# Kernel optimization log

Hardware: AMD Instinct MI355X
Metric: run time of the kernel (lower is better)

Reference implementation:

```python
import jax, jax.numpy as jnp
import numpy as np

N_M, N_D, E, D, H, O = 50000, 20000, 600000, 128, 128, 64


def _graph_conv(x_src, x_dst, src, dst, W_rel, b_rel, W_root, ew=None):
    # PyG GraphConv: lin_rel(scatter_add(msg)) + lin_root(x_dst)
    msg = x_src[src]                       # [E, d_src] gather
    if ew is not None:
        msg = msg * ew[:, None]            # edge-weighted messages
    agg = jax.ops.segment_sum(msg, dst, num_segments=x_dst.shape[0])  # [N_dst, d_src]
    return agg @ W_rel + b_rel + x_dst @ W_root


def setup_inputs() -> dict:
    key = jax.random.key(0)
    ks = jax.random.split(key, 16)
    s = 1.0 / np.sqrt(D)
    inp = {
        "x_meas": jax.random.normal(ks[0], (N_M, D), jnp.float32),
        "x_dem": jax.random.normal(ks[1], (N_D, D), jnp.float32),
        "src_m": jax.random.randint(ks[2], (E,), 0, N_M, jnp.int32),
        "dst_m": jax.random.randint(ks[3], (E,), 0, N_M, jnp.int32),
        "src_b": jax.random.randint(ks[4], (E,), 0, N_M, jnp.int32),
        "dst_b": jax.random.randint(ks[5], (E,), 0, N_D, jnp.int32),
        "edge_weight": jax.random.normal(ks[6], (E,), jnp.float32),
        "W_rel1": jax.random.normal(ks[7], (D, H), jnp.float32) * s,
        "b_rel1": jnp.zeros((H,), jnp.float32),
        "W_root1": jax.random.normal(ks[8], (D, H), jnp.float32) * s,
        "W_rel2": jax.random.normal(ks[9], (D, H), jnp.float32) * s,
        "b_rel2": jnp.zeros((H,), jnp.float32),
        "W_root2": jax.random.normal(ks[10], (D, H), jnp.float32) * s,
        "W_rel3": jax.random.normal(ks[11], (H, H), jnp.float32) * s,
        "b_rel3": jnp.zeros((H,), jnp.float32),
        "W_root3": jax.random.normal(ks[12], (H, H), jnp.float32) * s,
        "W_lin": jax.random.normal(ks[13], (H, O), jnp.float32) * (1.0 / np.sqrt(H)),
        "b_lin": jnp.zeros((O,), jnp.float32),
    }
    return inp


def reference(x_meas, x_dem, src_m, dst_m, src_b, dst_b, edge_weight,
              W_rel1, b_rel1, W_root1, W_rel2, b_rel2, W_root2,
              W_rel3, b_rel3, W_root3, W_lin, b_lin):
    ew = jax.nn.sigmoid(edge_weight)
    movie_x = jax.nn.relu(_graph_conv(x_meas, x_meas, src_m, dst_m, W_rel1, b_rel1, W_root1))
    user_x = jax.nn.relu(_graph_conv(x_meas, x_dem, src_b, dst_b, W_rel2, b_rel2, W_root2, ew))
    user_x = jax.nn.relu(_graph_conv(movie_x, user_x, src_b, dst_b, W_rel3, b_rel3, W_root3, ew))
    return user_x @ W_lin + b_lin  # [N_D, O]
```

## Files before the change

### kernel.cpp

```cpp
#include <hip/hip_runtime.h>


typedef unsigned short u16;
typedef unsigned int u32;
typedef __attribute__((ext_vector_type(8))) short bf16x8;
typedef __attribute__((ext_vector_type(4))) float f32x4;

#define NMC 50000
#define NDC 20000
#define EC  600000
#define CM  64
#define CD  32
#define CHM (EC / CM)
#define CHD (EC / CD)
#define NWM (NMC / 2)
#define NWD (NDC / 2)

__device__ __forceinline__ float bf2f(u16 h) {
    union { u32 u; float f; } v; v.u = ((u32)h) << 16; return v.f;
}
__device__ __forceinline__ u16 f2bf(float f) {
    union { float f; u32 u; } v; v.f = f;
    u32 lsb = (v.u >> 16) & 1u;
    v.u += 0x7fffu + lsb;
    return (u16)(v.u >> 16);
}

__global__ __launch_bounds__(256)
void hist_lds(const int* __restrict__ dst_m, const int* __restrict__ dst_b,
              int* __restrict__ rank_m, int* __restrict__ rank_b,
              u32* __restrict__ histm, u32* __restrict__ histd)
{
    __shared__ u32 h[NWM];
    const int b = blockIdx.x;
    const bool isM = b < CM;
    const int nw = isM ? NWM : NWD;
    for (int i = threadIdx.x; i < nw; i += 256) h[i] = 0;
    __syncthreads();
    if (isM) {
        const int e0 = b * CHM;
        const int e1 = min(EC, e0 + CHM);
        for (int e = e0 + threadIdx.x; e < e1; e += 256) {
            int d = dst_m[e];
            int sh = (d & 1) * 16;
            u32 old = atomicAdd(&h[d >> 1], 1u << sh);
            rank_m[e] = (old >> sh) & 0xffffu;
        }
        __syncthreads();
        for (int i = threadIdx.x; i < nw; i += 256)
            histm[(size_t)b * NWM + i] = h[i];
    } else {
        const int bb = b - CM;
        const int e0 = bb * CHD;
        const int e1 = min(EC, e0 + CHD);
        for (int e = e0 + threadIdx.x; e < e1; e += 256) {
            int d = dst_b[e];
            int sh = (d & 1) * 16;
            u32 old = atomicAdd(&h[d >> 1], 1u << sh);
            rank_b[e] = (old >> sh) & 0xffffu;
        }
        __syncthreads();
        for (int i = threadIdx.x; i < nw; i += 256)
            histd[(size_t)bb * NWD + i] = h[i];
    }
}

__global__ __launch_bounds__(256)
void prep2(const float* __restrict__ xm, u16* __restrict__ xm_bf, int n8m,
           const float* __restrict__ xd, u16* __restrict__ xd_bf, int n8d,
           const float* __restrict__ w0, const float* __restrict__ w1,
           const float* __restrict__ w2, const float* __restrict__ w3,
           const float* __restrict__ w4, const float* __restrict__ w5,
           const float* __restrict__ w6, u16* __restrict__ wbuf,
           int TB, int TB2)
{
    const int b = blockIdx.x;
    if (b < TB + TB2) {
        const bool isM = b < TB;
        const float* src = isM ? xm : xd;
        u16* dst = isM ? xm_bf : xd_bf;
        int n8 = isM ? n8m : n8d;
        int i = (b - (isM ? 0 : TB)) * 256 + threadIdx.x;
        if (i >= n8) return;
        float4 a = ((const float4*)src)[2 * i];
        float4 c2 = ((const float4*)src)[2 * i + 1];
        ushort4 h0; h0.x = f2bf(a.x); h0.y = f2bf(a.y); h0.z = f2bf(a.z); h0.w = f2bf(a.w);
        ushort4 h1; h1.x = f2bf(c2.x); h1.y = f2bf(c2.y); h1.z = f2bf(c2.z); h1.w = f2bf(c2.w);
        ((ushort4*)dst)[2 * i]     = h0;
        ((ushort4*)dst)[2 * i + 1] = h1;
    } else {
        int bb = b - TB - TB2;
        const int widx = bb >> 6;
        const int o    = ((bb & 63) << 8) + threadIdx.x;
        const int OC   = (widx == 6) ? 64 : 128;
        if (o >= OC * 128) return;
        const float* W;
        switch (widx) {
            case 0: W = w0; break; case 1: W = w1; break; case 2: W = w2; break;
            case 3: W = w3; break; case 4: W = w4; break; case 5: W = w5; break;
            default: W = w6;
        }
        int j = o & 7;
        int lane = (o >> 3) & 63;
        int n, c;
        if (OC == 128) { n = (o >> 9) & 7; c = o >> 12; }
        else           { n = (o >> 9) & 3; c = o >> 11; }
        int col = n * 16 + (lane & 15);
        int k   = c * 32 + (lane >> 4) * 8 + j;
        wbuf[widx * 16384 + o] = f2bf(W[k * OC + col]);
    }
}

__global__ __launch_bounds__(256)
void basescan2(u32* __restrict__ histm, u32* __restrict__ histd,
               int* __restrict__ deg_m, int* __restrict__ deg_b)
{
    int w = blockIdx.x * 256 + threadIdx.x;
    u32* hist; int* deg; int NW, C;
    if (w < NWM)            { hist = histm; deg = deg_m; NW = NWM; C = CM; }
    else if (w < NWM + NWD) { hist = histd; deg = deg_b; NW = NWD; C = CD; w -= NWM; }
    else return;
    u32 runlo = 0, runhi = 0;
    for (int c = 0; c < C; ++c) {
        u32 v = hist[(size_t)c * NW + w];
        hist[(size_t)c * NW + w] = runlo | (runhi << 16);
        runlo += v & 0xffffu;
        runhi += v >> 16;
    }
    deg[2 * w]     = (int)runlo;
    deg[2 * w + 1] = (int)runhi;
}

__device__ __forceinline__ int wave_incl_scan(int v, int lane) {
#pragma unroll
    for (int off = 1; off < 64; off <<= 1) {
        int t = __shfl_up(v, off, 64);
        if (lane >= off) v += t;
    }
    return v;
}

__global__ __launch_bounds__(1024)
void scan2_kernel(const int* __restrict__ degA, int* __restrict__ rpA, int nA,
                  const int* __restrict__ degB, int* __restrict__ rpB, int nB)
{
    const int* deg = blockIdx.x ? degB : degA;
    int* rp = blockIdx.x ? rpB : rpA;
    int n = blockIdx.x ? nB : nA;

    __shared__ int wsum[16];
    __shared__ int carry;
    const int tid = threadIdx.x, lane = tid & 63, wid = tid >> 6;
    if (tid == 0) carry = 0;
    __syncthreads();

    for (int base = 0; base < n; base += 4096) {
        int idx = base + tid * 4;
        int4 v = make_int4(0, 0, 0, 0);
        if (idx + 3 < n) v = *(const int4*)(deg + idx);
        else {
            if (idx + 0 < n) v.x = deg[idx + 0];
            if (idx + 1 < n) v.y = deg[idx + 1];
            if (idx + 2 < n) v.z = deg[idx + 2];
            if (idx + 3 < n) v.w = deg[idx + 3];
        }
        int s = v.x + v.y + v.z + v.w;
        int incl = wave_incl_scan(s, lane);
        if (lane == 63) wsum[wid] = incl;
        __syncthreads();
        if (wid == 0) {
            int t = (lane < 16) ? wsum[lane] : 0;
            int ti = wave_incl_scan(t, lane);
            if (lane < 16) wsum[lane] = ti - t;
        }
        __syncthreads();
        int base_t = carry + wsum[wid] + incl - s;
        if (idx + 3 < n) {
            int4 st;
            st.x = base_t;
            st.y = base_t + v.x;
            st.z = base_t + v.x + v.y;
            st.w = base_t + v.x + v.y + v.z;
            *(int4*)(rp + idx) = st;
        } else {
            if (idx + 0 < n) rp[idx + 0] = base_t;
            if (idx + 1 < n) rp[idx + 1] = base_t + v.x;
            if (idx + 2 < n) rp[idx + 2] = base_t + v.x + v.y;
            if (idx + 3 < n) rp[idx + 3] = base_t + v.x + v.y + v.z;
        }
        __syncthreads();
        if (tid == 1023) carry += wsum[15] + incl;
        __syncthreads();
    }
    if (tid == 0) rp[n] = carry;
}

__global__ __launch_bounds__(256)
void fill_kernel(const int* __restrict__ src_m, const int* __restrict__ dst_m,
                 const int* __restrict__ src_b, const int* __restrict__ dst_b,
                 const float* __restrict__ edge_w,
                 const int* __restrict__ rp_m, const int* __restrict__ rp_b,
                 const int* __restrict__ rank_m, const int* __restrict__ rank_b,
                 const u32* __restrict__ histm, const u32* __restrict__ histd,
                 int* __restrict__ srcs_m, int2* __restrict__ edges_b, int E)
{
    int t = blockIdx.x * 256 + threadIdx.x;
    if (t < E) {
        int d = dst_m[t];
        int c = t / CHM;
        u32 pk = histm[(size_t)c * NWM + (d >> 1)];
        int base = (pk >> ((d & 1) * 16)) & 0xffffu;
        int pos = rp_m[d] + base + rank_m[t];
        srcs_m[pos] = src_m[t];
    } else if (t < 2 * E) {
        int e = t - E;
        int d = dst_b[e];
        int c = e / CHD;
        u32 pkb = histd[(size_t)c * NWD + (d >> 1)];
        int base = (pkb >> ((d & 1) * 16)) & 0xffffu;
        int pos = rp_b[d] + base + rank_b[e];
        float x = edge_w[e];
        int2 pk;
        pk.x = src_b[e];
        pk.y = __float_as_int(1.0f / (1.0f + __expf(-x)));
        edges_b[pos] = pk;
    }
}

__global__ __launch_bounds__(256)
void gather12(const u16* __restrict__ Xb,
              const int* __restrict__ srcs_m, const int2* __restrict__ edges_b,
              const int* __restrict__ rp_m, const int* __restrict__ rp_b,
              u16* __restrict__ agg1, u16* __restrict__ agg2, int NM, int ND)
{
    const int h  = blockIdx.x * 8 + (threadIdx.x >> 5);
    const int cl = threadIdx.x & 31;
    float4 acc = make_float4(0.f, 0.f, 0.f, 0.f);

    if (h < NM) {
        int i   = rp_m[h];
        int end = rp_m[h + 1];
        for (; i + 4 <= end; i += 4) {
            int s0 = srcs_m[i], s1 = srcs_m[i + 1], s2 = srcs_m[i + 2], s3 = srcs_m[i + 3];
            ushort4 v0 = *(const ushort4*)(Xb + (size_t)s0 * 128 + cl * 4);
            ushort4 v1 = *(const ushort4*)(Xb + (size_t)s1 * 128 + cl * 4);
            ushort4 v2 = *(const ushort4*)(Xb + (size_t)s2 * 128 + cl * 4);
            ushort4 v3 = *(const ushort4*)(Xb + (size_t)s3 * 128 + cl * 4);
            acc.x += (bf2f(v0.x) + bf2f(v1.x)) + (bf2f(v2.x) + bf2f(v3.x));
            acc.y += (bf2f(v0.y) + bf2f(v1.y)) + (bf2f(v2.y) + bf2f(v3.y));
            acc.z += (bf2f(v0.z) + bf2f(v1.z)) + (bf2f(v2.z) + bf2f(v3.z));
            acc.w += (bf2f(v0.w) + bf2f(v1.w)) + (bf2f(v2.w) + bf2f(v3.w));
        }
        for (; i < end; ++i) {
            int s = srcs_m[i];
            ushort4 v = *(const ushort4*)(Xb + (size_t)s * 128 + cl * 4);
            acc.x += bf2f(v.x); acc.y += bf2f(v.y);
            acc.z += bf2f(v.z); acc.w += bf2f(v.w);
        }
        ushort4 st;
        st.x = f2bf(acc.x); st.y = f2bf(acc.y);
        st.z = f2bf(acc.z); st.w = f2bf(acc.w);
        *(ushort4*)(agg1 + (size_t)h * 128 + cl * 4) = st;
    } else if (h < NM + ND) {
        int node = h - NM;
        int i   = rp_b[node];
        int end = rp_b[node + 1];
        for (; i + 4 <= end; i += 4) {
            int2 p0 = edges_b[i],     p1 = edges_b[i + 1];
            int2 p2 = edges_b[i + 2], p3 = edges_b[i + 3];
            float w0 = __int_as_float(p0.y), w1 = __int_as_float(p1.y);
            float w2 = __int_as_float(p2.y), w3 = __int_as_float(p3.y);
            ushort4 v0 = *(const ushort4*)(Xb + (size_t)p0.x * 128 + cl * 4);
            ushort4 v1 = *(const ushort4*)(Xb + (size_t)p1.x * 128 + cl * 4);
            ushort4 v2 = *(const ushort4*)(Xb + (size_t)p2.x * 128 + cl * 4);
            ushort4 v3 = *(const ushort4*)(Xb + (size_t)p3.x * 128 + cl * 4);
            acc.x = fmaf(w0, bf2f(v0.x), acc.x); acc.y = fmaf(w0, bf2f(v0.y), acc.y);
            acc.z = fmaf(w0, bf2f(v0.z), acc.z); acc.w = fmaf(w0, bf2f(v0.w), acc.w);
            acc.x = fmaf(w1, bf2f(v1.x), acc.x); acc.y = fmaf(w1, bf2f(v1.y), acc.y);
            acc.z = fmaf(w1, bf2f(v1.z), acc.z); acc.w = fmaf(w1, bf2f(v1.w), acc.w);
            acc.x = fmaf(w2, bf2f(v2.x), acc.x); acc.y = fmaf(w2, bf2f(v2.y), acc.y);
            acc.z = fmaf(w2, bf2f(v2.z), acc.z); acc.w = fmaf(w2, bf2f(v2.w), acc.w);
            acc.x = fmaf(w3, bf2f(v3.x), acc.x); acc.y = fmaf(w3, bf2f(v3.y), acc.y);
            acc.z = fmaf(w3, bf2f(v3.z), acc.z); acc.w = fmaf(w3, bf2f(v3.w), acc.w);
        }
        for (; i < end; ++i) {
            int2 pk = edges_b[i];
            float w = __int_as_float(pk.y);
            ushort4 v = *(const ushort4*)(Xb + (size_t)pk.x * 128 + cl * 4);
            acc.x = fmaf(w, bf2f(v.x), acc.x); acc.y = fmaf(w, bf2f(v.y), acc.y);
            acc.z = fmaf(w, bf2f(v.z), acc.z); acc.w = fmaf(w, bf2f(v.w), acc.w);
        }
        ushort4 st;
        st.x = f2bf(acc.x); st.y = f2bf(acc.y);
        st.z = f2bf(acc.z); st.w = f2bf(acc.w);
        *(ushort4*)(agg2 + (size_t)node * 128 + cl * 4) = st;
    }
}

__global__ __launch_bounds__(256)
void gather3_kernel(const u16* __restrict__ Mv, const int2* __restrict__ edges_b,
                    const int* __restrict__ rp_b, u16* __restrict__ agg3, int ND)
{
    const int node = blockIdx.x * 8 + (threadIdx.x >> 5);
    if (node >= ND) return;
    const int cl = threadIdx.x & 31;
    int i   = rp_b[node];
    int end = rp_b[node + 1];

    float4 acc = make_float4(0.f, 0.f, 0.f, 0.f);
    for (; i + 4 <= end; i += 4) {
        int2 p0 = edges_b[i],     p1 = edges_b[i + 1];
        int2 p2 = edges_b[i + 2], p3 = edges_b[i + 3];
        float w0 = __int_as_float(p0.y), w1 = __int_as_float(p1.y);
        float w2 = __int_as_float(p2.y), w3 = __int_as_float(p3.y);
        ushort4 v0 = *(const ushort4*)(Mv + (size_t)p0.x * 128 + cl * 4);
        ushort4 v1 = *(const ushort4*)(Mv + (size_t)p1.x * 128 + cl * 4);
        ushort4 v2 = *(const ushort4*)(Mv + (size_t)p2.x * 128 + cl * 4);
        ushort4 v3 = *(const ushort4*)(Mv + (size_t)p3.x * 128 + cl * 4);
        acc.x = fmaf(w0, bf2f(v0.x), acc.x); acc.y = fmaf(w0, bf2f(v0.y), acc.y);
        acc.z = fmaf(w0, bf2f(v0.z), acc.z); acc.w = fmaf(w0, bf2f(v0.w), acc.w);
        acc.x = fmaf(w1, bf2f(v1.x), acc.x); acc.y = fmaf(w1, bf2f(v1.y), acc.y);
        acc.z = fmaf(w1, bf2f(v1.z), acc.z); acc.w = fmaf(w1, bf2f(v1.w), acc.w);
        acc.x = fmaf(w2, bf2f(v2.x), acc.x); acc.y = fmaf(w2, bf2f(v2.y), acc.y);
        acc.z = fmaf(w2, bf2f(v2.z), acc.z); acc.w = fmaf(w2, bf2f(v2.w), acc.w);
        acc.x = fmaf(w3, bf2f(v3.x), acc.x); acc.y = fmaf(w3, bf2f(v3.y), acc.y);
        acc.z = fmaf(w3, bf2f(v3.z), acc.z); acc.w = fmaf(w3, bf2f(v3.w), acc.w);
    }
    for (; i < end; ++i) {
        int2 pk = edges_b[i];
        float w = __int_as_float(pk.y);
        ushort4 v = *(const ushort4*)(Mv + (size_t)pk.x * 128 + cl * 4);
        acc.x = fmaf(w, bf2f(v.x), acc.x); acc.y = fmaf(w, bf2f(v.y), acc.y);
        acc.z = fmaf(w, bf2f(v.z), acc.z); acc.w = fmaf(w, bf2f(v.w), acc.w);
    }
    ushort4 st;
    st.x = f2bf(acc.x); st.y = f2bf(acc.y);
    st.z = f2bf(acc.z); st.w = f2bf(acc.w);
    *(ushort4*)(agg3 + (size_t)node * 128 + cl * 4) = st;
}

__global__ __launch_bounds__(256)
void conv12_mfma(const u16* __restrict__ agg1, const u16* __restrict__ w1r,
                 const float* __restrict__ b1, const u16* __restrict__ xm_bf,
                 const u16* __restrict__ w1o, u16* __restrict__ C1, int N1, int cb1,
                 const u16* __restrict__ agg2, const u16* __restrict__ w2r,
                 const float* __restrict__ b2, const u16* __restrict__ xd_bf,
                 const u16* __restrict__ w2o, u16* __restrict__ C2, int N2)
{
    __shared__ u16 sW[16384];

    const bool seg1 = (int)blockIdx.x < cb1;
    const u16 *A0, *A1p, *Wr, *Wo; const float* bias; u16* C; int N, base;
    if (seg1) { A0 = agg1; A1p = xm_bf; Wr = w1r; Wo = w1o; bias = b1; C = C1; N = N1; base = blockIdx.x; }
    else      { A0 = agg2; A1p = xd_bf; Wr = w2r; Wo = w2o; bias = b2; C = C2; N = N2; base = blockIdx.x - cb1; }

    const int tid  = threadIdx.x;
    const int lane = tid & 63;
    const int m0   = (base * 4 + (tid >> 6)) * 32;
    const int lr   = lane & 15;
    const int quad = lane >> 4;

    int r0 = m0 + lr;      if (r0 >= N) r0 = N - 1;
    int r1 = m0 + 16 + lr; if (r1 >= N) r1 = N - 1;

    f32x4 acc[2][8];
#pragma unroll
    for (int mt = 0; mt < 2; ++mt)
#pragma unroll
        for (int n = 0; n < 8; ++n) acc[mt][n] = (f32x4){0.f, 0.f, 0.f, 0.f};

    for (int i = tid; i < 2048; i += 256)
        ((uint4*)sW)[i] = ((const uint4*)Wr)[i];
    __syncthreads();
#pragma unroll
    for (int c = 0; c < 4; ++c) {
        const int kb = c * 32 + quad * 8;
        bf16x8 a0 = *(const bf16x8*)(A0 + (size_t)r0 * 128 + kb);
        bf16x8 a1 = *(const bf16x8*)(A0 + (size_t)r1 * 128 + kb);
        const u16* wp = sW + c * 4096 + lane * 8;
#pragma unroll
        for (int n = 0; n < 8; ++n) {
            bf16x8 b = *(const bf16x8*)(wp + n * 512);
            acc[0][n] = __builtin_amdgcn_mfma_f32_16x16x32_bf16(a0, b, acc[0][n], 0, 0, 0);
            acc[1][n] = __builtin_amdgcn_mfma_f32_16x16x32_bf16(a1, b, acc[1][n], 0, 0, 0);
        }
    }
    __syncthreads();

    for (int i = tid; i < 2048; i += 256)
        ((uint4*)sW)[i] = ((const uint4*)Wo)[i];
    __syncthreads();
#pragma unroll
    for (int c = 0; c < 4; ++c) {
        const int kb = c * 32 + quad * 8;
        bf16x8 a0 = *(const bf16x8*)(A1p + (size_t)r0 * 128 + kb);
        bf16x8 a1 = *(const bf16x8*)(A1p + (size_t)r1 * 128 + kb);
        const u16* wp = sW + c * 4096 + lane * 8;
#pragma unroll
        for (int n = 0; n < 8; ++n) {
            bf16x8 b = *(const bf16x8*)(wp + n * 512);
            acc[0][n] = __builtin_amdgcn_mfma_f32_16x16x32_bf16(a0, b, acc[0][n], 0, 0, 0);
            acc[1][n] = __builtin_amdgcn_mfma_f32_16x16x32_bf16(a1, b, acc[1][n], 0, 0, 0);
        }
    }

#pragma unroll
    for (int mt = 0; mt < 2; ++mt) {
#pragma unroll
        for (int n = 0; n < 8; ++n) {
            const int col = n * 16 + lr;
            const float b = bias[col];
#pragma unroll
            for (int r = 0; r < 4; ++r) {
                int row = m0 + mt * 16 + quad * 4 + r;
                if (row >= N) continue;
                C[(size_t)row * 128 + col] = f2bf(fmaxf(acc[mt][n][r] + b, 0.f));
            }
        }
    }
}

__global__ __launch_bounds__(256)
void conv3_lin(const u16* __restrict__ A1, const u16* __restrict__ Wr,
               const float* __restrict__ bias3,
               const u16* __restrict__ A2, const u16* __restrict__ Wo,
               const u16* __restrict__ Wl, const float* __restrict__ bias_l,
               float* __restrict__ out, int N)
{
    __shared__ u16 lds[17408 + 8192];
    u16* tile = lds;
    u16* sWl  = lds + 17408;

    const int tid  = threadIdx.x;
    const int lane = tid & 63;
    const int wv   = tid >> 6;
    const int wbase = wv * 32;
    const int m0   = (blockIdx.x * 4 + wv) * 32;
    const int lr   = lane & 15;
    const int quad = lane >> 4;

    int r0 = m0 + lr;      if (r0 >= N) r0 = N - 1;
    int r1 = m0 + 16 + lr; if (r1 >= N) r1 = N - 1;

    f32x4 acc[2][8];
#pragma unroll
    for (int mt = 0; mt < 2; ++mt)
#pragma unroll
        for (int n = 0; n < 8; ++n) acc[mt][n] = (f32x4){0.f, 0.f, 0.f, 0.f};

    for (int i = tid; i < 1024; i += 256)
        ((uint4*)sWl)[i] = ((const uint4*)Wl)[i];
    for (int i = tid; i < 2048; i += 256)
        ((uint4*)lds)[i] = ((const uint4*)Wr)[i];
    __syncthreads();
#pragma unroll
    for (int c = 0; c < 4; ++c) {
        const int kb = c * 32 + quad * 8;
        bf16x8 a0 = *(const bf16x8*)(A1 + (size_t)r0 * 128 + kb);
        bf16x8 a1 = *(const bf16x8*)(A1 + (size_t)r1 * 128 + kb);
        const u16* wp = lds + c * 4096 + lane * 8;
#pragma unroll
        for (int n = 0; n < 8; ++n) {
            bf16x8 b = *(const bf16x8*)(wp + n * 512);
            acc[0][n] = __builtin_amdgcn_mfma_f32_16x16x32_bf16(a0, b, acc[0][n], 0, 0, 0);
            acc[1][n] = __builtin_amdgcn_mfma_f32_16x16x32_bf16(a1, b, acc[1][n], 0, 0, 0);
        }
    }
    __syncthreads();
    for (int i = tid; i < 2048; i += 256)
        ((uint4*)lds)[i] = ((const uint4*)Wo)[i];
    __syncthreads();
#pragma unroll
    for (int c = 0; c < 4; ++c) {
        const int kb = c * 32 + quad * 8;
        bf16x8 a0 = *(const bf16x8*)(A2 + (size_t)r0 * 128 + kb);
        bf16x8 a1 = *(const bf16x8*)(A2 + (size_t)r1 * 128 + kb);
        const u16* wp = lds + c * 4096 + lane * 8;
#pragma unroll
        for (int n = 0; n < 8; ++n) {
            bf16x8 b = *(const bf16x8*)(wp + n * 512);
            acc[0][n] = __builtin_amdgcn_mfma_f32_16x16x32_bf16(a0, b, acc[0][n], 0, 0, 0);
            acc[1][n] = __builtin_amdgcn_mfma_f32_16x16x32_bf16(a1, b, acc[1][n], 0, 0, 0);
        }
    }
    __syncthreads();

#pragma unroll
    for (int mt = 0; mt < 2; ++mt) {
#pragma unroll
        for (int n = 0; n < 8; ++n) {
            const int col = n * 16 + lr;
            const float b = bias3[col];
#pragma unroll
            for (int r = 0; r < 4; ++r) {
                int row = wbase + mt * 16 + quad * 4 + r;
                tile[row * 136 + col] = f2bf(fmaxf(acc[mt][n][r] + b, 0.f));
            }
        }
    }
    __syncthreads();

    f32x4 acc2[2][4];
#pragma unroll
    for (int mt = 0; mt < 2; ++mt)
#pragma unroll
        for (int n = 0; n < 4; ++n) acc2[mt][n] = (f32x4){0.f, 0.f, 0.f, 0.f};

#pragma unroll
    for (int c = 0; c < 4; ++c) {
        const int kb = c * 32 + quad * 8;
        bf16x8 a0 = *(const bf16x8*)(tile + (wbase + lr) * 136 + kb);
        bf16x8 a1 = *(const bf16x8*)(tile + (wbase + 16 + lr) * 136 + kb);
#pragma unroll
        for (int n = 0; n < 4; ++n) {
            bf16x8 b = *(const bf16x8*)(sWl + c * 2048 + n * 512 + lane * 8);
            acc2[0][n] = __builtin_amdgcn_mfma_f32_16x16x32_bf16(a0, b, acc2[0][n], 0, 0, 0);
            acc2[1][n] = __builtin_amdgcn_mfma_f32_16x16x32_bf16(a1, b, acc2[1][n], 0, 0, 0);
        }
    }

#pragma unroll
    for (int mt = 0; mt < 2; ++mt) {
#pragma unroll
        for (int n = 0; n < 4; ++n) {
            const int col = n * 16 + lr;
            const float b = bias_l[col];
#pragma unroll
            for (int r = 0; r < 4; ++r) {
                int row = m0 + mt * 16 + quad * 4 + r;
                if (row >= N) continue;
                out[(size_t)row * 64 + col] = acc2[mt][n][r] + b;
            }
        }
    }
}

extern "C" void kernel_launch(void* const* d_in, const int* in_sizes, int n_in,
                              void* d_out, int out_size, void* d_ws, size_t ws_size,
                              hipStream_t stream)
{
    const float* x_meas  = (const float*)d_in[0];
    const float* x_dem   = (const float*)d_in[1];
    const int*   src_m   = (const int*)d_in[2];
    const int*   dst_m   = (const int*)d_in[3];
    const int*   src_b   = (const int*)d_in[4];
    const int*   dst_b   = (const int*)d_in[5];
    const float* edge_w  = (const float*)d_in[6];
    const float* W_rel1  = (const float*)d_in[7];
    const float* b_rel1  = (const float*)d_in[8];
    const float* W_root1 = (const float*)d_in[9];
    const float* W_rel2  = (const float*)d_in[10];
    const float* b_rel2  = (const float*)d_in[11];
    const float* W_root2 = (const float*)d_in[12];
    const float* W_rel3  = (const float*)d_in[13];
    const float* b_rel3  = (const float*)d_in[14];
    const float* W_root3 = (const float*)d_in[15];
    const float* W_lin   = (const float*)d_in[16];
    const float* b_lin   = (const float*)d_in[17];
    float* out = (float*)d_out;

    const int NM = NMC, ND = NDC, E = EC;

    char* p = (char*)d_ws;
    auto alloc = [&](size_t bytes) { char* r = p; p += (bytes + 511) & ~(size_t)511; return r; };
    u32*   histm   = (u32*)alloc((size_t)CM * NWM * 4);
    u32*   histd   = (u32*)alloc((size_t)CD * NWD * 4);
    int*   deg_m   = (int*)alloc((size_t)NM * 4);
    int*   deg_b   = (int*)alloc((size_t)ND * 4);
    int*   rp_m    = (int*)alloc((size_t)(NM + 1) * 4);
    int*   rp_b    = (int*)alloc((size_t)(ND + 1) * 4);
    int*   srcs_m  = (int*)alloc((size_t)E * 4);
    int2*  edges_b = (int2*)alloc((size_t)E * 8);
    u16*   agg1    = (u16*)alloc((size_t)NM * 128 * 2);
    u16*   agg2    = (u16*)alloc((size_t)ND * 128 * 2);
    u16*   movie   = (u16*)alloc((size_t)NM * 128 * 2);
    u16*   t2      = (u16*)alloc((size_t)ND * 128 * 2);
    u16*   xd_bf   = (u16*)alloc((size_t)ND * 128 * 2);
    u16*   wbuf    = (u16*)alloc(7 * 16384 * 2);
    int* rank_m = (int*)agg1;
    int* rank_b = rank_m + E;
    u16* xm_bf  = movie;
    u16* agg3   = agg1;

    const int TB  = (NM * 16 + 255) / 256;
    const int TB2 = (ND * 16 + 255) / 256;
    const int WB  = 448;
    const int HB  = (2 * E + 255) / 256;

    hist_lds<<<CM + CD, 256, 0, stream>>>(dst_m, dst_b, rank_m, rank_b, histm, histd);

    prep2<<<TB + TB2 + WB, 256, 0, stream>>>(
        x_meas, xm_bf, NM * 16, x_dem, xd_bf, ND * 16,
        W_rel1, W_root1, W_rel2, W_root2, W_rel3, W_root3, W_lin, wbuf,
        TB, TB2);

    basescan2<<<(NWM + NWD + 255) / 256, 256, 0, stream>>>(histm, histd, deg_m, deg_b);
    scan2_kernel<<<2, 1024, 0, stream>>>(deg_m, rp_m, NM, deg_b, rp_b, ND);
    fill_kernel<<<HB, 256, 0, stream>>>(src_m, dst_m, src_b, dst_b, edge_w,
                                        rp_m, rp_b, rank_m, rank_b,
                                        histm, histd, srcs_m, edges_b, E);

    gather12<<<(NM + ND + 7) / 8, 256, 0, stream>>>(xm_bf, srcs_m, edges_b,
                                                    rp_m, rp_b, agg1, agg2, NM, ND);

    const int cb1 = (NM + 127) / 128;
    const int cb2 = (ND + 127) / 128;
    u16* w1r = wbuf + 0 * 16384; u16* w1o = wbuf + 1 * 16384;
    u16* w2r = wbuf + 2 * 16384; u16* w2o = wbuf + 3 * 16384;
    u16* w3r = wbuf + 4 * 16384; u16* w3o = wbuf + 5 * 16384;
    u16* wl  = wbuf + 6 * 16384;
    conv12_mfma<<<cb1 + cb2, 256, 0, stream>>>(agg1, w1r, b_rel1, xm_bf, w1o, movie, NM, cb1,
                                               agg2, w2r, b_rel2, xd_bf, w2o, t2,    ND);

    gather3_kernel<<<(ND + 7) / 8, 256, 0, stream>>>(movie, edges_b, rp_b, agg3, ND);

    conv3_lin<<<cb2, 256, 0, stream>>>(agg3, w3r, b_rel3, t2, w3o, wl, b_lin, out, ND);
}
```

Measured before the change: 303.4 us.

## Merge CSR base-scan, prefix scan and fill into one cooperative kernel

```diff
diff --git a/kernel.cpp b/kernel.cpp
--- a/kernel.cpp
+++ b/kernel.cpp
@@ -1,5 +1,8 @@
 #include <hip/hip_runtime.h>
-
+#include <hip/hip_cooperative_groups.h>
+
+
+namespace cg = cooperative_groups;
 
 typedef unsigned short u16;
 typedef unsigned int u32;
@@ -15,6 +18,8 @@
 #define CHD (EC / CD)
 #define NWM (NMC / 2)
 #define NWD (NDC / 2)
+#define CGRID 1536
+#define CTHREADS (CGRID * 256)
 
 __device__ __forceinline__ float bf2f(u16 h) {
     union { u32 u; float f; } v; v.u = ((u32)h) << 16; return v.f;
@@ -111,27 +116,7 @@
     }
 }
 
-__global__ __launch_bounds__(256)
-void basescan2(u32* __restrict__ histm, u32* __restrict__ histd,
-               int* __restrict__ deg_m, int* __restrict__ deg_b)
-{
-    int w = blockIdx.x * 256 + threadIdx.x;
-    u32* hist; int* deg; int NW, C;
-    if (w < NWM)            { hist = histm; deg = deg_m; NW = NWM; C = CM; }
-    else if (w < NWM + NWD) { hist = histd; deg = deg_b; NW = NWD; C = CD; w -= NWM; }
-    else return;
-    u32 runlo = 0, runhi = 0;
-    for (int c = 0; c < C; ++c) {
-        u32 v = hist[(size_t)c * NW + w];
-        hist[(size_t)c * NW + w] = runlo | (runhi << 16);
-        runlo += v & 0xffffu;
-        runhi += v >> 16;
-    }
-    deg[2 * w]     = (int)runlo;
-    deg[2 * w + 1] = (int)runhi;
-}
-
-__device__ __forceinline__ int wave_incl_scan(int v, int lane) {
+__device__ __forceinline__ int wave_incl_scan64(int v, int lane) {
 #pragma unroll
     for (int off = 1; off < 64; off <<= 1) {
         int t = __shfl_up(v, off, 64);
@@ -140,90 +125,139 @@
     return v;
 }
 
-__global__ __launch_bounds__(1024)
-void scan2_kernel(const int* __restrict__ degA, int* __restrict__ rpA, int nA,
-                  const int* __restrict__ degB, int* __restrict__ rpB, int nB)
+__global__ __launch_bounds__(256)
+void coop_csr(u32* __restrict__ histm, u32* __restrict__ histd,
+              int* __restrict__ deg_m, int* __restrict__ deg_b,
+              int* __restrict__ rp_m, int* __restrict__ rp_b,
+              int* __restrict__ pm, int* __restrict__ pd,
+              const int* __restrict__ src_m, const int* __restrict__ dst_m,
+              const int* __restrict__ src_b, const int* __restrict__ dst_b,
+              const float* __restrict__ edge_w,
+              const int* __restrict__ rank_m, const int* __restrict__ rank_b,
+              int* __restrict__ srcs_m, int2* __restrict__ edges_b)
 {
-    const int* deg = blockIdx.x ? degB : degA;
-    int* rp = blockIdx.x ? rpB : rpA;
-    int n = blockIdx.x ? nB : nA;
-
-    __shared__ int wsum[16];
-    __shared__ int carry;
-    const int tid = threadIdx.x, lane = tid & 63, wid = tid >> 6;
-    if (tid == 0) carry = 0;
-    __syncthreads();
-
-    for (int base = 0; base < n; base += 4096) {
-        int idx = base + tid * 4;
-        int4 v = make_int4(0, 0, 0, 0);
-        if (idx + 3 < n) v = *(const int4*)(deg + idx);
-        else {
-            if (idx + 0 < n) v.x = deg[idx + 0];
-            if (idx + 1 < n) v.y = deg[idx + 1];
-            if (idx + 2 < n) v.z = deg[idx + 2];
-            if (idx + 3 < n) v.w = deg[idx + 3];
-        }
+    cg::grid_group grid = cg::this_grid();
+    const int tid = threadIdx.x;
+    const int b   = blockIdx.x;
+    const int gt  = b * 256 + tid;
+    __shared__ int ws[8];
+
+    for (int w = gt; w < NWM + NWD; w += CTHREADS) {
+        u32* hist; int* deg; int NW, C; int ww = w;
+        if (ww < NWM) { hist = histm; deg = deg_m; NW = NWM; C = CM; }
+        else          { hist = histd; deg = deg_b; NW = NWD; C = CD; ww -= NWM; }
+        u32 runlo = 0, runhi = 0;
+        for (int c = 0; c < C; ++c) {
+            u32 v = hist[(size_t)c * NW + ww];
+            hist[(size_t)c * NW + ww] = runlo | (runhi << 16);
+            runlo += v & 0xffffu;
+            runhi += v >> 16;
+        }
+        deg[2 * ww]     = (int)runlo;
+        deg[2 * ww + 1] = (int)runhi;
+    }
+    grid.sync();
+
+    if (b < 1024) {
+        int n0 = b * 49;
+        int v = 0;
+        if (tid < 49 && n0 + tid < NMC) v = deg_m[n0 + tid];
+        if (tid < 64) {
+#pragma unroll
+            for (int off = 32; off; off >>= 1) v += __shfl_down(v, off, 64);
+            if (tid == 0) pm[b] = v;
+        }
+    } else {
+        int bb = b - 1024;
+        int n0 = bb * 40;
+        int v = 0;
+        if (tid < 40 && n0 + tid < NDC) v = deg_b[n0 + tid];
+        if (tid < 64) {
+#pragma unroll
+            for (int off = 32; off; off >>= 1) v += __shfl_down(v, off, 64);
+            if (tid == 0) pd[bb] = v;
+        }
+    }
+    grid.sync();
+
+    if (b == 0) {
+        int4 v = *(const int4*)(pm + tid * 4);
         int s = v.x + v.y + v.z + v.w;
-        int incl = wave_incl_scan(s, lane);
-        if (lane == 63) wsum[wid] = incl;
+        int lane = tid & 63, wid = tid >> 6;
+        int incl = wave_incl_scan64(s, lane);
+        if (lane == 63) ws[wid] = incl;
         __syncthreads();
-        if (wid == 0) {
-            int t = (lane < 16) ? wsum[lane] : 0;
-            int ti = wave_incl_scan(t, lane);
-            if (lane < 16) wsum[lane] = ti - t;
+        if (tid == 0) {
+            int a0 = ws[0], a1 = ws[1], a2 = ws[2], a3 = ws[3];
+            ws[4] = 0; ws[5] = a0; ws[6] = a0 + a1; ws[7] = a0 + a1 + a2;
+            rp_m[NMC] = a0 + a1 + a2 + a3;
         }
         __syncthreads();
-        int base_t = carry + wsum[wid] + incl - s;
-        if (idx + 3 < n) {
-            int4 st;
-            st.x = base_t;
-            st.y = base_t + v.x;
-            st.z = base_t + v.x + v.y;
-            st.w = base_t + v.x + v.y + v.z;
-            *(int4*)(rp + idx) = st;
+        int base = ws[4 + wid] + incl - s;
+        pm[tid * 4 + 0] = base;
+        pm[tid * 4 + 1] = base + v.x;
+        pm[tid * 4 + 2] = base + v.x + v.y;
+        pm[tid * 4 + 3] = base + v.x + v.y + v.z;
+    } else if (b == 1) {
+        int2 v = *(const int2*)(pd + tid * 2);
+        int s = v.x + v.y;
+        int lane = tid & 63, wid = tid >> 6;
+        int incl = wave_incl_scan64(s, lane);
+        if (lane == 63) ws[wid] = incl;
+        __syncthreads();
+        if (tid == 0) {
+            int a0 = ws[0], a1 = ws[1], a2 = ws[2], a3 = ws[3];
+            ws[4] = 0; ws[5] = a0; ws[6] = a0 + a1; ws[7] = a0 + a1 + a2;
+            rp_b[NDC] = a0 + a1 + a2 + a3;
+        }
+        __syncthreads();
+        int base = ws[4 + wid] + incl - s;
+        pd[tid * 2 + 0] = base;
+        pd[tid * 2 + 1] = base + v.x;
+    }
+    grid.sync();
+
+    if (b < 1024) {
+        int n0 = b * 49;
+        int v = 0;
+        if (tid < 49 && n0 + tid < NMC) v = deg_m[n0 + tid];
+        if (tid < 64) {
+            int incl = wave_incl_scan64(v, tid);
+            if (tid < 49 && n0 + tid < NMC) rp_m[n0 + tid] = pm[b] + incl - v;
+        }
+    } else {
+        int bb = b - 1024;
+        int n0 = bb * 40;
+        int v = 0;
+        if (tid < 40 && n0 + tid < NDC) v = deg_b[n0 + tid];
+        if (tid < 64) {
+            int incl = wave_incl_scan64(v, tid);
+            if (tid < 40 && n0 + tid < NDC) rp_b[n0 + tid] = pd[bb] + incl - v;
+        }
+    }
+    grid.sync();
+
+    for (int t = gt; t < 2 * EC; t += CTHREADS) {
+        if (t < EC) {
+            int d = dst_m[t];
+            int c = t / CHM;
+            u32 pk = histm[(size_t)c * NWM + (d >> 1)];
+            int base = (pk >> ((d & 1) * 16)) & 0xffffu;
+            int pos = rp_m[d] + base + rank_m[t];
+            srcs_m[pos] = src_m[t];
         } else {
-            if (idx + 0 < n) rp[idx + 0] = base_t;
-            if (idx + 1 < n) rp[idx + 1] = base_t + v.x;
-            if (idx + 2 < n) rp[idx + 2] = base_t + v.x + v.y;
-            if (idx + 3 < n) rp[idx + 3] = base_t + v.x + v.y + v.z;
-        }
-        __syncthreads();
-        if (tid == 1023) carry += wsum[15] + incl;
-        __syncthreads();
-    }
-    if (tid == 0) rp[n] = carry;
-}
-
-__global__ __launch_bounds__(256)
-void fill_kernel(const int* __restrict__ src_m, const int* __restrict__ dst_m,
-                 const int* __restrict__ src_b, const int* __restrict__ dst_b,
-                 const float* __restrict__ edge_w,
-                 const int* __restrict__ rp_m, const int* __restrict__ rp_b,
-                 const int* __restrict__ rank_m, const int* __restrict__ rank_b,
-                 const u32* __restrict__ histm, const u32* __restrict__ histd,
-                 int* __restrict__ srcs_m, int2* __restrict__ edges_b, int E)
-{
-    int t = blockIdx.x * 256 + threadIdx.x;
-    if (t < E) {
-        int d = dst_m[t];
-        int c = t / CHM;
-        u32 pk = histm[(size_t)c * NWM + (d >> 1)];
-        int base = (pk >> ((d & 1) * 16)) & 0xffffu;
-        int pos = rp_m[d] + base + rank_m[t];
-        srcs_m[pos] = src_m[t];
-    } else if (t < 2 * E) {
-        int e = t - E;
-        int d = dst_b[e];
-        int c = e / CHD;
-        u32 pkb = histd[(size_t)c * NWD + (d >> 1)];
-        int base = (pkb >> ((d & 1) * 16)) & 0xffffu;
-        int pos = rp_b[d] + base + rank_b[e];
-        float x = edge_w[e];
-        int2 pk;
-        pk.x = src_b[e];
-        pk.y = __float_as_int(1.0f / (1.0f + __expf(-x)));
-        edges_b[pos] = pk;
+            int e = t - EC;
+            int d = dst_b[e];
+            int c = e / CHD;
+            u32 pkb = histd[(size_t)c * NWD + (d >> 1)];
+            int base = (pkb >> ((d & 1) * 16)) & 0xffffu;
+            int pos = rp_b[d] + base + rank_b[e];
+            float x = edge_w[e];
+            int2 pk;
+            pk.x = src_b[e];
+            pk.y = __float_as_int(1.0f / (1.0f + __expf(-x)));
+            edges_b[pos] = pk;
+        }
     }
 }
 
@@ -240,6 +274,26 @@
     if (h < NM) {
         int i   = rp_m[h];
         int end = rp_m[h + 1];
+        for (; i + 8 <= end; i += 8) {
+            int s0 = srcs_m[i+0], s1 = srcs_m[i+1], s2 = srcs_m[i+2], s3 = srcs_m[i+3];
+            int s4 = srcs_m[i+4], s5 = srcs_m[i+5], s6 = srcs_m[i+6], s7 = srcs_m[i+7];
+            ushort4 v0 = *(const ushort4*)(Xb + (size_t)s0 * 128 + cl * 4);
+            ushort4 v1 = *(const ushort4*)(Xb + (size_t)s1 * 128 + cl * 4);
+            ushort4 v2 = *(const ushort4*)(Xb + (size_t)s2 * 128 + cl * 4);
+            ushort4 v3 = *(const ushort4*)(Xb + (size_t)s3 * 128 + cl * 4);
+            ushort4 v4 = *(const ushort4*)(Xb + (size_t)s4 * 128 + cl * 4);
+            ushort4 v5 = *(const ushort4*)(Xb + (size_t)s5 * 128 + cl * 4);
+            ushort4 v6 = *(const ushort4*)(Xb + (size_t)s6 * 128 + cl * 4);
+            ushort4 v7 = *(const ushort4*)(Xb + (size_t)s7 * 128 + cl * 4);
+            acc.x += ((bf2f(v0.x)+bf2f(v1.x)) + (bf2f(v2.x)+bf2f(v3.x)))
+                   + ((bf2f(v4.x)+bf2f(v5.x)) + (bf2f(v6.x)+bf2f(v7.x)));
+            acc.y += ((bf2f(v0.y)+bf2f(v1.y)) + (bf2f(v2.y)+bf2f(v3.y)))
+                   + ((bf2f(v4.y)+bf2f(v5.y)) + (bf2f(v6.y)+bf2f(v7.y)));
+            acc.z += ((bf2f(v0.z)+bf2f(v1.z)) + (bf2f(v2.z)+bf2f(v3.z)))
+                   + ((bf2f(v4.z)+bf2f(v5.z)) + (bf2f(v6.z)+bf2f(v7.z)));
+            acc.w += ((bf2f(v0.w)+bf2f(v1.w)) + (bf2f(v2.w)+bf2f(v3.w)))
+                   + ((bf2f(v4.w)+bf2f(v5.w)) + (bf2f(v6.w)+bf2f(v7.w)));
+        }
         for (; i + 4 <= end; i += 4) {
             int s0 = srcs_m[i], s1 = srcs_m[i + 1], s2 = srcs_m[i + 2], s3 = srcs_m[i + 3];
             ushort4 v0 = *(const ushort4*)(Xb + (size_t)s0 * 128 + cl * 4);
@@ -265,6 +319,38 @@
         int node = h - NM;
         int i   = rp_b[node];
         int end = rp_b[node + 1];
+        for (; i + 8 <= end; i += 8) {
+            int2 p0 = edges_b[i+0], p1 = edges_b[i+1], p2 = edges_b[i+2], p3 = edges_b[i+3];
+            int2 p4 = edges_b[i+4], p5 = edges_b[i+5], p6 = edges_b[i+6], p7 = edges_b[i+7];
+            ushort4 v0 = *(const ushort4*)(Xb + (size_t)p0.x * 128 + cl * 4);
+            ushort4 v1 = *(const ushort4*)(Xb + (size_t)p1.x * 128 + cl * 4);
+            ushort4 v2 = *(const ushort4*)(Xb + (size_t)p2.x * 128 + cl * 4);
+            ushort4 v3 = *(const ushort4*)(Xb + (size_t)p3.x * 128 + cl * 4);
+            ushort4 v4 = *(const ushort4*)(Xb + (size_t)p4.x * 128 + cl * 4);
+            ushort4 v5 = *(const ushort4*)(Xb + (size_t)p5.x * 128 + cl * 4);
+            ushort4 v6 = *(const ushort4*)(Xb + (size_t)p6.x * 128 + cl * 4);
+            ushort4 v7 = *(const ushort4*)(Xb + (size_t)p7.x * 128 + cl * 4);
+            float w0 = __int_as_float(p0.y), w1 = __int_as_float(p1.y);
+            float w2 = __int_as_float(p2.y), w3 = __int_as_float(p3.y);
+            float w4 = __int_as_float(p4.y), w5 = __int_as_float(p5.y);
+            float w6 = __int_as_float(p6.y), w7 = __int_as_float(p7.y);
+            acc.x = fmaf(w0, bf2f(v0.x), acc.x); acc.y = fmaf(w0, bf2f(v0.y), acc.y);
+            acc.z = fmaf(w0, bf2f(v0.z), acc.z); acc.w = fmaf(w0, bf2f(v0.w), acc.w);
+            acc.x = fmaf(w1, bf2f(v1.x), acc.x); acc.y = fmaf(w1, bf2f(v1.y), acc.y);
+            acc.z = fmaf(w1, bf2f(v1.z), acc.z); acc.w = fmaf(w1, bf2f(v1.w), acc.w);
+            acc.x = fmaf(w2, bf2f(v2.x), acc.x); acc.y = fmaf(w2, bf2f(v2.y), acc.y);
+            acc.z = fmaf(w2, bf2f(v2.z), acc.z); acc.w = fmaf(w2, bf2f(v2.w), acc.w);
+            acc.x = fmaf(w3, bf2f(v3.x), acc.x); acc.y = fmaf(w3, bf2f(v3.y), acc.y);
+            acc.z = fmaf(w3, bf2f(v3.z), acc.z); acc.w = fmaf(w3, bf2f(v3.w), acc.w);
+            acc.x = fmaf(w4, bf2f(v4.x), acc.x); acc.y = fmaf(w4, bf2f(v4.y), acc.y);
+            acc.z = fmaf(w4, bf2f(v4.z), acc.z); acc.w = fmaf(w4, bf2f(v4.w), acc.w);
+            acc.x = fmaf(w5, bf2f(v5.x), acc.x); acc.y = fmaf(w5, bf2f(v5.y), acc.y);
+            acc.z = fmaf(w5, bf2f(v5.z), acc.z); acc.w = fmaf(w5, bf2f(v5.w), acc.w);
+            acc.x = fmaf(w6, bf2f(v6.x), acc.x); acc.y = fmaf(w6, bf2f(v6.y), acc.y);
+            acc.z = fmaf(w6, bf2f(v6.z), acc.z); acc.w = fmaf(w6, bf2f(v6.w), acc.w);
+            acc.x = fmaf(w7, bf2f(v7.x), acc.x); acc.y = fmaf(w7, bf2f(v7.y), acc.y);
+            acc.z = fmaf(w7, bf2f(v7.z), acc.z); acc.w = fmaf(w7, bf2f(v7.w), acc.w);
+        }
         for (; i + 4 <= end; i += 4) {
             int2 p0 = edges_b[i],     p1 = edges_b[i + 1];
             int2 p2 = edges_b[i + 2], p3 = edges_b[i + 3];
@@ -308,6 +394,38 @@
     int end = rp_b[node + 1];
 
     float4 acc = make_float4(0.f, 0.f, 0.f, 0.f);
+    for (; i + 8 <= end; i += 8) {
+        int2 p0 = edges_b[i+0], p1 = edges_b[i+1], p2 = edges_b[i+2], p3 = edges_b[i+3];
+        int2 p4 = edges_b[i+4], p5 = edges_b[i+5], p6 = edges_b[i+6], p7 = edges_b[i+7];
+        ushort4 v0 = *(const ushort4*)(Mv + (size_t)p0.x * 128 + cl * 4);
+        ushort4 v1 = *(const ushort4*)(Mv + (size_t)p1.x * 128 + cl * 4);
+        ushort4 v2 = *(const ushort4*)(Mv + (size_t)p2.x * 128 + cl * 4);
+        ushort4 v3 = *(const ushort4*)(Mv + (size_t)p3.x * 128 + cl * 4);
+        ushort4 v4 = *(const ushort4*)(Mv + (size_t)p4.x * 128 + cl * 4);
+        ushort4 v5 = *(const ushort4*)(Mv + (size_t)p5.x * 128 + cl * 4);
+        ushort4 v6 = *(const ushort4*)(Mv + (size_t)p6.x * 128 + cl * 4);
+        ushort4 v7 = *(const ushort4*)(Mv + (size_t)p7.x * 128 + cl * 4);
+        float w0 = __int_as_float(p0.y), w1 = __int_as_float(p1.y);
+        float w2 = __int_as_float(p2.y), w3 = __int_as_float(p3.y);
+        float w4 = __int_as_float(p4.y), w5 = __int_as_float(p5.y);
+        float w6 = __int_as_float(p6.y), w7 = __int_as_float(p7.y);
+        acc.x = fmaf(w0, bf2f(v0.x), acc.x); acc.y = fmaf(w0, bf2f(v0.y), acc.y);
+        acc.z = fmaf(w0, bf2f(v0.z), acc.z); acc.w = fmaf(w0, bf2f(v0.w), acc.w);
+        acc.x = fmaf(w1, bf2f(v1.x), acc.x); acc.y = fmaf(w1, bf2f(v1.y), acc.y);
+        acc.z = fmaf(w1, bf2f(v1.z), acc.z); acc.w = fmaf(w1, bf2f(v1.w), acc.w);
+        acc.x = fmaf(w2, bf2f(v2.x), acc.x); acc.y = fmaf(w2, bf2f(v2.y), acc.y);
+        acc.z = fmaf(w2, bf2f(v2.z), acc.z); acc.w = fmaf(w2, bf2f(v2.w), acc.w);
+        acc.x = fmaf(w3, bf2f(v3.x), acc.x); acc.y = fmaf(w3, bf2f(v3.y), acc.y);
+        acc.z = fmaf(w3, bf2f(v3.z), acc.z); acc.w = fmaf(w3, bf2f(v3.w), acc.w);
+        acc.x = fmaf(w4, bf2f(v4.x), acc.x); acc.y = fmaf(w4, bf2f(v4.y), acc.y);
+        acc.z = fmaf(w4, bf2f(v4.z), acc.z); acc.w = fmaf(w4, bf2f(v4.w), acc.w);
+        acc.x = fmaf(w5, bf2f(v5.x), acc.x); acc.y = fmaf(w5, bf2f(v5.y), acc.y);
+        acc.z = fmaf(w5, bf2f(v5.z), acc.z); acc.w = fmaf(w5, bf2f(v5.w), acc.w);
+        acc.x = fmaf(w6, bf2f(v6.x), acc.x); acc.y = fmaf(w6, bf2f(v6.y), acc.y);
+        acc.z = fmaf(w6, bf2f(v6.z), acc.z); acc.w = fmaf(w6, bf2f(v6.w), acc.w);
+        acc.x = fmaf(w7, bf2f(v7.x), acc.x); acc.y = fmaf(w7, bf2f(v7.y), acc.y);
+        acc.z = fmaf(w7, bf2f(v7.z), acc.z); acc.w = fmaf(w7, bf2f(v7.w), acc.w);
+    }
     for (; i + 4 <= end; i += 4) {
         int2 p0 = edges_b[i],     p1 = edges_b[i + 1];
         int2 p2 = edges_b[i + 2], p3 = edges_b[i + 3];
@@ -569,6 +687,8 @@
     int*   deg_b   = (int*)alloc((size_t)ND * 4);
     int*   rp_m    = (int*)alloc((size_t)(NM + 1) * 4);
     int*   rp_b    = (int*)alloc((size_t)(ND + 1) * 4);
+    int*   pm      = (int*)alloc(1024 * 4);
+    int*   pd      = (int*)alloc(512 * 4);
     int*   srcs_m  = (int*)alloc((size_t)E * 4);
     int2*  edges_b = (int2*)alloc((size_t)E * 8);
     u16*   agg1    = (u16*)alloc((size_t)NM * 128 * 2);
@@ -585,7 +705,6 @@
     const int TB  = (NM * 16 + 255) / 256;
     const int TB2 = (ND * 16 + 255) / 256;
     const int WB  = 448;
-    const int HB  = (2 * E + 255) / 256;
 
     hist_lds<<<CM + CD, 256, 0, stream>>>(dst_m, dst_b, rank_m, rank_b, histm, histd);
 
@@ -594,11 +713,14 @@
         W_rel1, W_root1, W_rel2, W_root2, W_rel3, W_root3, W_lin, wbuf,
         TB, TB2);
 
-    basescan2<<<(NWM + NWD + 255) / 256, 256, 0, stream>>>(histm, histd, deg_m, deg_b);
-    scan2_kernel<<<2, 1024, 0, stream>>>(deg_m, rp_m, NM, deg_b, rp_b, ND);
-    fill_kernel<<<HB, 256, 0, stream>>>(src_m, dst_m, src_b, dst_b, edge_w,
-                                        rp_m, rp_b, rank_m, rank_b,
-                                        histm, histd, srcs_m, edges_b, E);
+    {
+        void* args[] = { &histm, &histd, &deg_m, &deg_b, &rp_m, &rp_b, &pm, &pd,
+                         (void*)&src_m, (void*)&dst_m, (void*)&src_b, (void*)&dst_b,
+                         (void*)&edge_w, (void*)&rank_m, (void*)&rank_b,
+                         &srcs_m, &edges_b };
+        hipLaunchCooperativeKernel((void*)coop_csr, dim3(CGRID), dim3(256),
+                                   args, 0, stream);
+    }
 
     gather12<<<(NM + ND + 7) / 8, 256, 0, stream>>>(xm_bf, srcs_m, edges_b,
                                                     rp_m, rp_b, agg1, agg2, NM, ND);
```

After: 856.1 us. 2.82x slower.
